# Kernel tuning notes

Hardware: AMD Instinct MI355X
Metric: run time of the kernel (lower is better)

Reference implementation:

```python
import jax, jax.numpy as jnp
import numpy as np

B, N = 64, 4096
D_IN, D_SLOT, K, N_ITER, MLP_H = 128, 128, 8, 3, 256
EPS = 1e-8
LN_EPS = 1e-5  # torch LayerNorm default


def layer_norm(x, g, b):
    m = jnp.mean(x, axis=-1, keepdims=True)
    v = jnp.mean((x - m) ** 2, axis=-1, keepdims=True)
    return (x - m) * jax.lax.rsqrt(v + LN_EPS) * g + b


def setup_inputs() -> dict:
    key = jax.random.key(0)
    ks = jax.random.split(key, 12)
    s = D_SLOT ** -0.5
    return {
        "inputs": jax.random.normal(ks[0], (B, N, D_IN), jnp.float32),
        "noise": jax.random.normal(ks[1], (B, K, D_SLOT), jnp.float32),
        "ln_in_g": jnp.ones((D_IN,), jnp.float32),
        "ln_in_b": jnp.zeros((D_IN,), jnp.float32),
        "ln_sl_g": jnp.ones((D_SLOT,), jnp.float32),
        "ln_sl_b": jnp.zeros((D_SLOT,), jnp.float32),
        "ln_mlp_g": jnp.ones((D_SLOT,), jnp.float32),
        "ln_mlp_b": jnp.zeros((D_SLOT,), jnp.float32),
        "slots_mu": jax.random.normal(ks[2], (1, 1, D_SLOT), jnp.float32) * s,
        "slots_log_sigma": jnp.zeros((1, 1, D_SLOT), jnp.float32),
        "Wq": jax.random.normal(ks[3], (D_SLOT, D_SLOT), jnp.float32) * s,
        "Wk": jax.random.normal(ks[4], (D_SLOT, D_IN), jnp.float32) * s,
        "Wv": jax.random.normal(ks[5], (D_SLOT, D_IN), jnp.float32) * s,
        "gru_Wih": jax.random.normal(ks[6], (3 * D_SLOT, D_SLOT), jnp.float32) * s,
        "gru_Whh": jax.random.normal(ks[7], (3 * D_SLOT, D_SLOT), jnp.float32) * s,
        "gru_bih": jnp.zeros((3 * D_SLOT,), jnp.float32),
        "gru_bhh": jnp.zeros((3 * D_SLOT,), jnp.float32),
        "mlp_W1": jax.random.normal(ks[8], (MLP_H, D_SLOT), jnp.float32) * s,
        "mlp_b1": jnp.zeros((MLP_H,), jnp.float32),
        "mlp_W2": jax.random.normal(ks[9], (D_SLOT, MLP_H), jnp.float32) * (MLP_H ** -0.5),
        "mlp_b2": jnp.zeros((D_SLOT,), jnp.float32),
    }


def gru_cell(x, h, Wih, Whh, bih, bhh):
    # torch GRUCell: gate order r, z, n
    gx = x @ Wih.T + bih
    gh = h @ Whh.T + bhh
    xr, xz, xn = jnp.split(gx, 3, axis=-1)
    hr, hz, hn = jnp.split(gh, 3, axis=-1)
    r = jax.nn.sigmoid(xr + hr)
    z = jax.nn.sigmoid(xz + hz)
    n = jnp.tanh(xn + r * hn)
    return (1.0 - z) * n + z * h


def reference(inputs, noise, ln_in_g, ln_in_b, ln_sl_g, ln_sl_b, ln_mlp_g, ln_mlp_b,
              slots_mu, slots_log_sigma, Wq, Wk, Wv,
              gru_Wih, gru_Whh, gru_bih, gru_bhh,
              mlp_W1, mlp_b1, mlp_W2, mlp_b2):
    # init slots: mu + sigma * eps
    slots = slots_mu + jnp.exp(slots_log_sigma) * noise  # (B, K, d)
    x = layer_norm(inputs, ln_in_g, ln_in_b)
    k = jnp.einsum('bnd,ed->bne', x, Wk)  # (B, N, d_slot)
    v = jnp.einsum('bnd,ed->bne', x, Wv)
    scale = D_SLOT ** -0.5
    attn = None
    for _ in range(N_ITER):
        slots_prev = slots
        s_n = layer_norm(slots, ln_sl_g, ln_sl_b)
        q = jnp.einsum('bkd,ed->bke', s_n, Wq)
        dots = jnp.einsum('bkd,bnd->bkn', q, k) * scale
        attn = jax.nn.softmax(dots, axis=1)  # competitive: softmax over slots
        attn_normed = attn / (jnp.sum(attn, axis=-1, keepdims=True) + EPS)
        updates = jnp.einsum('bkn,bnd->bkd', attn_normed, v)
        slots = gru_cell(updates.reshape(-1, D_SLOT), slots_prev.reshape(-1, D_SLOT),
                         gru_Wih, gru_Whh, gru_bih, gru_bhh).reshape(B, K, D_SLOT)
        h = layer_norm(slots, ln_mlp_g, ln_mlp_b)
        h = jax.nn.gelu(h @ mlp_W1.T + mlp_b1, approximate=False)
        slots = slots + h @ mlp_W2.T + mlp_b2
    return slots, attn
```

## Files before the change

kernel.cpp:

```cpp
#include <hip/hip_runtime.h>
#include <hip/hip_bf16.h>
#include <math.h>

typedef unsigned int u32;
typedef unsigned long long u64;
typedef unsigned short u16;
typedef __bf16 bf16x8 __attribute__((ext_vector_type(8)));
typedef float f32x4 __attribute__((ext_vector_type(4)));

#define DEV __device__ __forceinline__

DEV u32 bfr(float f){ u32 u = __float_as_uint(f); return (u + 0x7fffu + ((u>>16)&1u)) >> 16; }
DEV u16 b1v(float a){ return __builtin_bit_cast(u16, (__bf16)a); }
DEV u32 pk2(float a, float b){
  return (u32)__builtin_bit_cast(u16, (__bf16)a) | ((u32)__builtin_bit_cast(u16, (__bf16)b) << 16);
}
DEV float red32(float v){
  v += __shfl_xor(v,1); v += __shfl_xor(v,2); v += __shfl_xor(v,4);
  v += __shfl_xor(v,8); v += __shfl_xor(v,16); return v;
}

__global__ void kInitSlots(const float* __restrict__ noise, const float* __restrict__ mu,
                           const float* __restrict__ ls, float* __restrict__ slots){
  int i4 = blockIdx.x*256 + threadIdx.x;
  int d4 = i4 & 31;
  float4 nv = ((const float4*)noise)[i4];
  float4 mv = ((const float4*)mu)[d4];
  float4 lv = ((const float4*)ls)[d4];
  float4 r;
  r.x = mv.x + expf(lv.x)*nv.x;
  r.y = mv.y + expf(lv.y)*nv.y;
  r.z = mv.z + expf(lv.z)*nv.z;
  r.w = mv.w + expf(lv.w)*nv.w;
  ((float4*)slots)[i4] = r;
}

__global__ void kInitW(const float* __restrict__ Wk, const float* __restrict__ Wv,
                       const float* __restrict__ g, const float* __restrict__ bb,
                       u16* __restrict__ wg, float* __restrict__ c1, float* __restrict__ c2){
  int e = threadIdx.x;
  const float4* src = (const float4*)((e < 128) ? (Wk + e*128) : (Wv + (e-128)*128));
  float a1 = 0.f, a2 = 0.f;
  #pragma unroll
  for (int d4 = 0; d4 < 32; ++d4){
    float4 wv = src[d4];
    float4 gv = ((const float4*)g)[d4];
    float4 bv = ((const float4*)bb)[d4];
    a1 += wv.x*gv.x + wv.y*gv.y + wv.z*gv.z + wv.w*gv.w;
    a2 += wv.x*bv.x + wv.y*bv.y + wv.z*bv.z + wv.w*bv.w;
    u32 w0 = bfr(wv.x*gv.x) | (bfr(wv.y*gv.y) << 16);
    u32 w1 = bfr(wv.z*gv.z) | (bfr(wv.w*gv.w) << 16);
    *(uint2*)&wg[e*128 + d4*4] = make_uint2(w0, w1);
  }
  c1[e] = a1; c2[e] = a2;
}

__global__ void kInitT(const float* __restrict__ Wih, const float* __restrict__ Whh,
                       const float* __restrict__ W1, const float* __restrict__ W2,
                       float2* __restrict__ gruT, float* __restrict__ w1T, float* __restrict__ w2T){
  int i = blockIdx.x*256 + threadIdx.x;
  if (i < 49152){
    int d = i / 384, g = i - d*384;
    gruT[i] = make_float2(Wih[g*128 + d], Whh[g*128 + d]);
  } else if (i < 81920){
    int j = i - 49152;
    int d = j >> 8, h = j & 255;
    w1T[j] = W1[h*128 + d];
  } else if (i < 114688){
    int q = i - 81920;
    int j = q >> 7, d = q & 127;
    w2T[q] = W2[d*256 + j];
  }
}

__global__ __launch_bounds__(512, 2) void kA(const float* __restrict__ x,
    const u16* __restrict__ wg, const float* __restrict__ c1g, const float* __restrict__ c2g,
    u16* __restrict__ kbuf, u16* __restrict__ vbuf)
{
  __shared__ __align__(16) u16 sWg[128*128];
  __shared__ __align__(16) u16 sE[8*16*128];
  __shared__ float sC1[128], sC2[128];
  const int t = threadIdx.x, l = t & 63, w = t >> 6;
  const int bid = blockIdx.x;
  const int half = (bid >> 3) & 1;
  const int rowgroup = (bid & 7)*32 + (bid >> 4);
  const int rowbase = rowgroup * 1024;

  const uint4* wg4 = (const uint4*)wg;
  #pragma unroll
  for (int p = 0; p < 4; ++p){
    int G = t + p*512;
    int row = G >> 4, g = G & 15;
    uint4 v = wg4[(half*128 + row)*16 + g];
    *(uint4*)&sWg[row*128 + ((g ^ (row & 7)) << 3)] = v;
  }
  if (t < 128){ sC1[t] = c1g[half*128 + t]; sC2[t] = c2g[half*128 + t]; }
  __syncthreads();

  u16* dstbuf = half ? vbuf : kbuf;
  const float4* x4 = (const float4*)x;

  #pragma unroll 1
  for (int s = 0; s < 8; ++s){
    const int r0 = rowbase + s*128 + w*16;
    const int myrow = r0 + (l & 15);
    float s1 = 0.f, s2 = 0.f;
    uint4 af[4];
    #pragma unroll
    for (int kt = 0; kt < 4; ++kt){
      int g = kt*4 + (l >> 4);
      float4 A = x4[(size_t)myrow*32 + g*2];
      float4 B = x4[(size_t)myrow*32 + g*2 + 1];
      s1 += A.x + A.y + A.z + A.w + B.x + B.y + B.z + B.w;
      s2 += A.x*A.x + A.y*A.y + A.z*A.z + A.w*A.w
          + B.x*B.x + B.y*B.y + B.z*B.z + B.w*B.w;
      af[kt].x = pk2(A.x, A.y);
      af[kt].y = pk2(A.z, A.w);
      af[kt].z = pk2(B.x, B.y);
      af[kt].w = pk2(B.z, B.w);
    }
    s1 += __shfl_xor(s1, 16); s2 += __shfl_xor(s2, 16);
    s1 += __shfl_xor(s1, 32); s2 += __shfl_xor(s2, 32);
    float m = s1 * 0.0078125f;
    float rstd = rsqrtf(s2 * 0.0078125f - m*m + 1e-5f);
    f32x4 acc[8];
    #pragma unroll
    for (int c_ = 0; c_ < 8; ++c_) acc[c_] = (f32x4){0.f,0.f,0.f,0.f};
    #pragma unroll
    for (int ct = 0; ct < 8; ++ct){
      uint4 bf[4];
      #pragma unroll
      for (int kt = 0; kt < 4; ++kt){
        int wr = ct*16 + (l & 15);
        int g = kt*4 + (l >> 4);
        bf[kt] = *(const uint4*)&sWg[wr*128 + ((g ^ (wr & 7)) << 3)];
      }
      #pragma unroll
      for (int kt = 0; kt < 4; ++kt)
        acc[ct] = __builtin_amdgcn_mfma_f32_16x16x32_bf16(
            __builtin_bit_cast(bf16x8, af[kt]),
            __builtin_bit_cast(bf16x8, bf[kt]),
            acc[ct], 0, 0, 0);
    }
    float mvp[4], rvp[4];
    #pragma unroll
    for (int r = 0; r < 4; ++r){
      int rl = (l >> 4)*4 + r;
      mvp[r] = __shfl(m, rl);
      rvp[r] = __shfl(rstd, rl);
    }
    #pragma unroll
    for (int ct = 0; ct < 8; ++ct){
      int col = ct*16 + (l & 15);
      float c1v = sC1[col], c2v = sC2[col];
      #pragma unroll
      for (int r = 0; r < 4; ++r){
        int rl = (l >> 4)*4 + r;
        float valf = rvp[r]*(acc[ct][r] - mvp[r]*c1v) + c2v;
        int gran = (col >> 3) ^ (rl & 7);
        sE[w*2048 + rl*128 + (gran << 3) + (col & 7)] = b1v(valf);
      }
    }
    uint4* dst4 = (uint4*)dstbuf;
    #pragma unroll
    for (int p = 0; p < 4; ++p){
      int fl = l + p*64;
      int nl = fl >> 4, gb = fl & 15;
      uint4 v = *(const uint4*)&sE[w*2048 + nl*128 + ((gb ^ (nl & 7)) << 3)];
      dst4[(size_t)(r0 + nl)*16 + gb] = v;
    }
  }
}

__global__ __launch_bounds__(256) void kQ(const float* __restrict__ slots,
    const float* __restrict__ Wq, const float* __restrict__ lng, const float* __restrict__ lnb,
    uint4* __restrict__ qg)
{
  const int b = blockIdx.x, t = threadIdx.x;
  const int k8 = t >> 5, q32 = t & 31;
  __shared__ __align__(16) float sSn[1024];
  __shared__ __align__(16) float sQ[1024];
  {
    float4 sv = ((const float4*)slots)[b*256 + t];
    float s  = sv.x + sv.y + sv.z + sv.w;
    float ss = sv.x*sv.x + sv.y*sv.y + sv.z*sv.z + sv.w*sv.w;
    s = red32(s); ss = red32(ss);
    float m = s*0.0078125f, var = ss*0.0078125f - m*m;
    float rstd = rsqrtf(var + 1e-5f);
    float4 gv = ((const float4*)lng)[q32], bv = ((const float4*)lnb)[q32];
    float4 sn;
    sn.x = (sv.x - m)*rstd*gv.x + bv.x;
    sn.y = (sv.y - m)*rstd*gv.y + bv.y;
    sn.z = (sv.z - m)*rstd*gv.z + bv.z;
    sn.w = (sv.w - m)*rstd*gv.w + bv.w;
    *(float4*)&sSn[t*4] = sn;
  }
  __syncthreads();
  {
    const float4* Wq4 = (const float4*)Wq;
    #pragma unroll
    for (int i = 0; i < 4; ++i){
      int e = i*32 + q32;
      float acc = 0.f;
      #pragma unroll
      for (int d4 = 0; d4 < 32; ++d4){
        float4 qs = *(const float4*)&sSn[k8*128 + d4*4];
        float4 wv = Wq4[e*32 + d4];
        acc = fmaf(qs.x,wv.x,acc); acc = fmaf(qs.y,wv.y,acc);
        acc = fmaf(qs.z,wv.z,acc); acc = fmaf(qs.w,wv.w,acc);
      }
      sQ[k8*128 + e] = acc * 0.08838834764831845f;
    }
  }
  __syncthreads();
  if (t < 128){
    int slot = t >> 4, g = t & 15;
    const float* src = &sQ[slot*128 + g*8];
    uint4 o;
    o.x = pk2(src[0], src[1]); o.y = pk2(src[2], src[3]);
    o.z = pk2(src[4], src[5]); o.w = pk2(src[6], src[7]);
    qg[(b*8 + slot)*16 + g] = o;
  }
}

__global__ __launch_bounds__(256) void kB(const u16* __restrict__ kbuf,
   const u16* __restrict__ vbuf, const uint4* __restrict__ qg,
   float* __restrict__ part, float* __restrict__ attn_out, int write_attn,
   int cshift, int ntiles)
{
  const int t = threadIdx.x;
  const int b = blockIdx.x >> cshift, chunk = blockIdx.x & ((1 << cshift) - 1);
  const int w = t >> 6, l = t & 63;
  __shared__ __align__(16) u16 sVT[128*64];
  __shared__ __align__(16) u16 sAttnB[16*64];
  __shared__ float sRsP[32];

  uint4 qf[4];
  {
    int slot = l & 15;
    uint4 z = make_uint4(0,0,0,0);
    qf[0] = z; qf[1] = z; qf[2] = z; qf[3] = z;
    if (slot < 8){
      const uint4* qb = qg + ((size_t)b*8 + slot)*16 + (l >> 4);
      #pragma unroll
      for (int kt = 0; kt < 4; ++kt) qf[kt] = qb[kt*4];
    }
  }

  f32x4 accPV0 = (f32x4){0.f,0.f,0.f,0.f};
  f32x4 accPV1 = (f32x4){0.f,0.f,0.f,0.f};
  float rs = 0.f;
  const int myrow = w*16 + (l & 15);
  const size_t base = (size_t)b*4096 + (size_t)chunk*(ntiles*64);

  uint4 kf[4];
  {
    const u16* kr = kbuf + (base + myrow)*128;
    #pragma unroll
    for (int kt = 0; kt < 4; ++kt) kf[kt] = *(const uint4*)(kr + (kt*4 + (l >> 4))*8);
  }

  #pragma unroll 1
  for (int tile = 0; tile < ntiles; ++tile){
    const int n0 = tile*64;
    uint4 vld[4];
    {
      const uint4* vg = (const uint4*)(vbuf + (base + n0)*128);
      #pragma unroll
      for (int p = 0; p < 4; ++p) vld[p] = vg[t + p*256];
    }
    f32x4 dacc = (f32x4){0.f,0.f,0.f,0.f};
    #pragma unroll
    for (int kt = 0; kt < 4; ++kt)
      dacc = __builtin_amdgcn_mfma_f32_16x16x32_bf16(
          __builtin_bit_cast(bf16x8, kf[kt]),
          __builtin_bit_cast(bf16x8, qf[kt]), dacc, 0, 0, 0);
    if (tile < ntiles - 1){
      const u16* kr = kbuf + (base + n0 + 64 + myrow)*128;
      #pragma unroll
      for (int kt = 0; kt < 4; ++kt) kf[kt] = *(const uint4*)(kr + (kt*4 + (l >> 4))*8);
    }
    float at[4];
    #pragma unroll
    for (int r = 0; r < 4; ++r){
      float d = dacc[r];
      float mx = fmaxf(d, __shfl_xor(d, 1));
      mx = fmaxf(mx, __shfl_xor(mx, 2));
      mx = fmaxf(mx, __shfl_xor(mx, 4));
      float e = expf(d - mx);
      float ssum = e + __shfl_xor(e, 1);
      ssum += __shfl_xor(ssum, 2);
      ssum += __shfl_xor(ssum, 4);
      at[r] = e / ssum;
      rs += at[r];
    }
    {
      int slot = l & 15;
      int nb = w*16 + (l >> 4)*4;
      int g = (nb >> 3) ^ (slot & 7);
      *(u64*)((char*)sAttnB + slot*128 + (g << 4) + ((nb & 7) << 1)) =
          ((u64)pk2(at[2], at[3]) << 32) | (u64)pk2(at[0], at[1]);
    }
    #pragma unroll
    for (int p = 0; p < 4; ++p){
      int fl = t + p*256;
      int nl = fl >> 4, gb = fl & 15;
      u32 arr[4] = {vld[p].x, vld[p].y, vld[p].z, vld[p].w};
      #pragma unroll
      for (int h = 0; h < 4; ++h){
        #pragma unroll
        for (int e2 = 0; e2 < 2; ++e2){
          int e = h*2 + e2;
          int d = gb*8 + e;
          int g = (nl >> 3) ^ (d & 7) ^ (gb & 7);
          *(u16*)((char*)sVT + d*128 + (g << 4) + ((nl & 7) << 1)) =
              (u16)(e2 ? (arr[h] >> 16) : (arr[h] & 0xffffu));
        }
      }
    }
    __syncthreads();
    #pragma unroll
    for (int step = 0; step < 2; ++step){
      uint4 paf;
      {
        int slot = l & 15;
        int g = (step*4 + (l >> 4)) ^ (slot & 7);
        paf = *(const uint4*)((const char*)sAttnB + slot*128 + (g << 4));
      }
      #pragma unroll
      for (int ct = 0; ct < 2; ++ct){
        int d = w*32 + ct*16 + (l & 15);
        int g = (step*4 + (l >> 4)) ^ (d & 7) ^ ((d >> 3) & 7);
        uint4 pbf = *(const uint4*)((const char*)sVT + d*128 + (g << 4));
        if (ct == 0)
          accPV0 = __builtin_amdgcn_mfma_f32_16x16x32_bf16(
              __builtin_bit_cast(bf16x8, paf), __builtin_bit_cast(bf16x8, pbf), accPV0, 0,0,0);
        else
          accPV1 = __builtin_amdgcn_mfma_f32_16x16x32_bf16(
              __builtin_bit_cast(bf16x8, paf), __builtin_bit_cast(bf16x8, pbf), accPV1, 0,0,0);
      }
    }
    if (write_attn && (l & 15) < 8){
      #pragma unroll
      for (int r = 0; r < 4; ++r)
        attn_out[(size_t)(b*8 + (l & 15))*4096 + chunk*(ntiles*64) + n0 + w*16 + (l >> 4)*4 + r] = at[r];
    }
    __syncthreads();
  }

  float* pb = part + (size_t)blockIdx.x*1040;
  if ((l >> 4) < 2){
    #pragma unroll
    for (int r = 0; r < 4; ++r){
      int slot = (l >> 4)*4 + r;
      pb[slot*128 + w*32 + (l & 15)] = accPV0[r];
      pb[slot*128 + w*32 + 16 + (l & 15)] = accPV1[r];
    }
  }
  rs += __shfl_xor(rs, 16);
  rs += __shfl_xor(rs, 32);
  if (l < 8) sRsP[w*8 + l] = rs;
  __syncthreads();
  if (t < 8) pb[1024 + t] = sRsP[t] + sRsP[8 + t] + sRsP[16 + t] + sRsP[24 + t];
}

__global__ __launch_bounds__(384) void kC(const float* __restrict__ part,
  float* __restrict__ slots, const float2* __restrict__ gruT,
  const float* __restrict__ bih, const float* __restrict__ bhh,
  const float* __restrict__ lng, const float* __restrict__ lnb,
  const float* __restrict__ w1T, const float* __restrict__ b1,
  const float* __restrict__ w2T, const float* __restrict__ b2,
  float* __restrict__ out_slots, int last, int nchunk)
{
  const int t = threadIdx.x;
  const int r = blockIdx.x, b = r >> 3, k = r & 7;
  __shared__ float sU[128], sS[128], sG1[384], sG2[384];
  __shared__ float sNew[128], sH[128], sH1[256];
  __shared__ float sP[4];

  if (t < 128){
    float rs = 1e-8f;
    for (int c = 0; c < nchunk; ++c) rs += part[(size_t)(b*nchunk + c)*1040 + 1024 + k];
    float u = 0.f;
    for (int c = 0; c < nchunk; ++c) u += part[(size_t)(b*nchunk + c)*1040 + k*128 + t];
    sU[t] = u / rs;
    sS[t] = slots[r*128 + t];
  }
  __syncthreads();

  {
    float acc1 = bih[t], acc2 = bhh[t];
    #pragma unroll 8
    for (int d = 0; d < 128; ++d){
      float2 w = gruT[d*384 + t];
      float ud = sU[d], sd = sS[d];
      acc1 = fmaf(ud, w.x, acc1);
      acc2 = fmaf(sd, w.y, acc2);
    }
    sG1[t] = acc1; sG2[t] = acc2;
  }
  __syncthreads();

  if (t < 128){
    float rr = 1.f/(1.f + expf(-(sG1[t] + sG2[t])));
    float zz = 1.f/(1.f + expf(-(sG1[128 + t] + sG2[128 + t])));
    float nn = tanhf(sG1[256 + t] + rr*sG2[256 + t]);
    sNew[t] = (1.f - zz)*nn + zz*sS[t];
  }
  __syncthreads();
  if (t < 128){
    float v = sNew[t];
    float s = v, ss = v*v;
    s  += __shfl_xor(s,1);  ss += __shfl_xor(ss,1);
    s  += __shfl_xor(s,2);  ss += __shfl_xor(ss,2);
    s  += __shfl_xor(s,4);  ss += __shfl_xor(ss,4);
    s  += __shfl_xor(s,8);  ss += __shfl_xor(ss,8);
    s  += __shfl_xor(s,16); ss += __shfl_xor(ss,16);
    s  += __shfl_xor(s,32); ss += __shfl_xor(ss,32);
    if ((t & 63) == 0){ sP[(t >> 6)*2] = s; sP[(t >> 6)*2 + 1] = ss; }
  }
  __syncthreads();
  if (t < 128){
    float s = sP[0] + sP[2], ss = sP[1] + sP[3];
    float m = s*0.0078125f, var = ss*0.0078125f - m*m;
    float rstd = rsqrtf(var + 1e-5f);
    sH[t] = (sNew[t] - m)*rstd*lng[t] + lnb[t];
  }
  __syncthreads();

  if (t < 256){
    float acc = b1[t];
    #pragma unroll 8
    for (int d = 0; d < 128; ++d)
      acc = fmaf(sH[d], w1T[d*256 + t], acc);
    sH1[t] = 0.5f*acc*(1.f + erff(acc*0.70710678118654752f));
  }
  __syncthreads();

  if (t < 128){
    float acc = b2[t];
    #pragma unroll 8
    for (int j = 0; j < 256; ++j)
      acc = fmaf(sH1[j], w2T[j*128 + t], acc);
    float res = sNew[t] + acc;
    slots[r*128 + t] = res;
    if (last) out_slots[r*128 + t] = res;
  }
}

extern "C" void kernel_launch(void* const* d_in, const int* in_sizes, int n_in,
                              void* d_out, int out_size, void* d_ws, size_t ws_size,
                              hipStream_t stream)
{
  const float* inputs   = (const float*)d_in[0];
  const float* noise    = (const float*)d_in[1];
  const float* ln_in_g  = (const float*)d_in[2];
  const float* ln_in_b  = (const float*)d_in[3];
  const float* ln_sl_g  = (const float*)d_in[4];
  const float* ln_sl_b  = (const float*)d_in[5];
  const float* ln_mlp_g = (const float*)d_in[6];
  const float* ln_mlp_b = (const float*)d_in[7];
  const float* slots_mu = (const float*)d_in[8];
  const float* slots_ls = (const float*)d_in[9];
  const float* Wq  = (const float*)d_in[10];
  const float* Wk  = (const float*)d_in[11];
  const float* Wv  = (const float*)d_in[12];
  const float* Wih = (const float*)d_in[13];
  const float* Whh = (const float*)d_in[14];
  const float* bih = (const float*)d_in[15];
  const float* bhh = (const float*)d_in[16];
  const float* W1  = (const float*)d_in[17];
  const float* b1  = (const float*)d_in[18];
  const float* W2  = (const float*)d_in[19];
  const float* b2  = (const float*)d_in[20];
  float* out = (float*)d_out;

  char* ws = (char*)d_ws;
  u16*   kbuf  = (u16*)ws;
  u16*   vbuf  = (u16*)(ws + 67108864);
  float* slots = (float*)(ws + 134217728);
  u16*   wg    = (u16*)(ws + 134479872);
  float* c1    = (float*)(ws + 134545408);
  float* c2    = (float*)(ws + 134546432);
  float* part  = (float*)(ws + 134547456);

  int cshift, nchunk;
  {
    size_t need16 = 134547456ull + 16ull*64*1040*4 + 393216 + 131072 + 131072 + 131072;
    if (ws_size >= need16){ cshift = 4; nchunk = 16; }
    else                  { cshift = 3; nchunk = 8;  }
  }
  size_t partB = (size_t)nchunk*64*1040*4;
  float2* gruT = (float2*)(ws + 134547456 + partB);
  float*  w1T  = (float*)(ws + 134547456 + partB + 393216);
  float*  w2T  = (float*)(ws + 134547456 + partB + 393216 + 131072);
  uint4*  qg   = (uint4*)(ws + 134547456 + partB + 393216 + 262144);
  int ntiles = 64 / nchunk;

  kInitSlots<<<64, 256, 0, stream>>>(noise, slots_mu, slots_ls, slots);
  kInitW<<<1, 256, 0, stream>>>(Wk, Wv, ln_in_g, ln_in_b, wg, c1, c2);
  kInitT<<<448, 256, 0, stream>>>(Wih, Whh, W1, W2, gruT, w1T, w2T);
  kA<<<512, 512, 0, stream>>>(inputs, wg, c1, c2, kbuf, vbuf);
  for (int it = 0; it < 3; ++it){
    kQ<<<64, 256, 0, stream>>>(slots, Wq, ln_sl_g, ln_sl_b, qg);
    kB<<<64*nchunk, 256, 0, stream>>>(kbuf, vbuf, qg, part, out + 65536,
                                      it == 2, cshift, ntiles);
    kC<<<512, 384, 0, stream>>>(part, slots, gruT, bih, bhh,
                                ln_mlp_g, ln_mlp_b, w1T, b1, w2T, b2, out, it == 2, nchunk);
  }
}
```

Measured before the change: 342.1 us.

## Fuse next-iteration query projection into kC, prefetch V tiles, split kA blocks

kA now runs twice as many blocks, each handling half of a rowgroup's sub-tiles, to raise parallelism. kB prefetches the next V tile into registers alongside the next K tile and moves the attention writes before the barrier. kC now also computes the LayerNorm and Wq projection for the next iteration's queries, removing two of the three kQ launches. The costs are more register pressure in kB, a per-row Wq read in each kC block, and kA reloading its weight tile twice as often.

```diff
diff --git a/kernel.cpp b/kernel.cpp
--- a/kernel.cpp
+++ b/kernel.cpp
@@ -83,7 +83,8 @@
   const int t = threadIdx.x, l = t & 63, w = t >> 6;
   const int bid = blockIdx.x;
   const int half = (bid >> 3) & 1;
-  const int rowgroup = (bid & 7)*32 + (bid >> 4);
+  const int sub  = (bid >> 4) & 1;
+  const int rowgroup = (bid & 7)*32 + (bid >> 5);
   const int rowbase = rowgroup * 1024;
 
   const uint4* wg4 = (const uint4*)wg;
@@ -101,7 +102,7 @@
   const float4* x4 = (const float4*)x;
 
   #pragma unroll 1
-  for (int s = 0; s < 8; ++s){
+  for (int s = sub*4; s < sub*4 + 4; ++s){
     const int r0 = rowbase + s*128 + w*16;
     const int myrow = r0 + (l & 15);
     float s1 = 0.f, s2 = 0.f;
@@ -253,32 +254,33 @@
   const int myrow = w*16 + (l & 15);
   const size_t base = (size_t)b*4096 + (size_t)chunk*(ntiles*64);
 
-  uint4 kf[4];
+  uint4 kf[4], vld[4];
   {
     const u16* kr = kbuf + (base + myrow)*128;
     #pragma unroll
     for (int kt = 0; kt < 4; ++kt) kf[kt] = *(const uint4*)(kr + (kt*4 + (l >> 4))*8);
+    const uint4* vg = (const uint4*)(vbuf + base*128);
+    #pragma unroll
+    for (int p = 0; p < 4; ++p) vld[p] = vg[t + p*256];
   }
 
   #pragma unroll 1
   for (int tile = 0; tile < ntiles; ++tile){
     const int n0 = tile*64;
-    uint4 vld[4];
-    {
-      const uint4* vg = (const uint4*)(vbuf + (base + n0)*128);
-      #pragma unroll
-      for (int p = 0; p < 4; ++p) vld[p] = vg[t + p*256];
-    }
     f32x4 dacc = (f32x4){0.f,0.f,0.f,0.f};
     #pragma unroll
     for (int kt = 0; kt < 4; ++kt)
       dacc = __builtin_amdgcn_mfma_f32_16x16x32_bf16(
           __builtin_bit_cast(bf16x8, kf[kt]),
           __builtin_bit_cast(bf16x8, qf[kt]), dacc, 0, 0, 0);
+    uint4 vldN[4];
     if (tile < ntiles - 1){
       const u16* kr = kbuf + (base + n0 + 64 + myrow)*128;
       #pragma unroll
       for (int kt = 0; kt < 4; ++kt) kf[kt] = *(const uint4*)(kr + (kt*4 + (l >> 4))*8);
+      const uint4* vg = (const uint4*)(vbuf + (base + n0 + 64)*128);
+      #pragma unroll
+      for (int p = 0; p < 4; ++p) vldN[p] = vg[t + p*256];
     }
     float at[4];
     #pragma unroll
@@ -318,6 +320,11 @@
         }
       }
     }
+    if (write_attn && (l & 15) < 8){
+      #pragma unroll
+      for (int r = 0; r < 4; ++r)
+        attn_out[(size_t)(b*8 + (l & 15))*4096 + chunk*(ntiles*64) + n0 + w*16 + (l >> 4)*4 + r] = at[r];
+    }
     __syncthreads();
     #pragma unroll
     for (int step = 0; step < 2; ++step){
@@ -340,12 +347,11 @@
               __builtin_bit_cast(bf16x8, paf), __builtin_bit_cast(bf16x8, pbf), accPV1, 0,0,0);
       }
     }
-    if (write_attn && (l & 15) < 8){
-      #pragma unroll
-      for (int r = 0; r < 4; ++r)
-        attn_out[(size_t)(b*8 + (l & 15))*4096 + chunk*(ntiles*64) + n0 + w*16 + (l >> 4)*4 + r] = at[r];
-    }
     __syncthreads();
+    if (tile < ntiles - 1){
+      #pragma unroll
+      for (int p = 0; p < 4; ++p) vld[p] = vldN[p];
+    }
   }
 
   float* pb = part + (size_t)blockIdx.x*1040;
@@ -370,6 +376,8 @@
   const float* __restrict__ lng, const float* __restrict__ lnb,
   const float* __restrict__ w1T, const float* __restrict__ b1,
   const float* __restrict__ w2T, const float* __restrict__ b2,
+  const float* __restrict__ lnslg, const float* __restrict__ lnslb,
+  const float* __restrict__ Wq, uint4* __restrict__ qg,
   float* __restrict__ out_slots, int last, int nchunk)
 {
   const int t = threadIdx.x;
@@ -437,14 +445,59 @@
   }
   __syncthreads();
 
+  float res = 0.f;
   if (t < 128){
     float acc = b2[t];
     #pragma unroll 8
     for (int j = 0; j < 256; ++j)
       acc = fmaf(sH1[j], w2T[j*128 + t], acc);
-    float res = sNew[t] + acc;
+    res = sNew[t] + acc;
     slots[r*128 + t] = res;
     if (last) out_slots[r*128 + t] = res;
+  }
+  if (last) return;
+
+  __syncthreads();
+  if (t < 128) sH[t] = res;
+  __syncthreads();
+  if (t < 128){
+    float v = sH[t];
+    float s = v, ss = v*v;
+    s  += __shfl_xor(s,1);  ss += __shfl_xor(ss,1);
+    s  += __shfl_xor(s,2);  ss += __shfl_xor(ss,2);
+    s  += __shfl_xor(s,4);  ss += __shfl_xor(ss,4);
+    s  += __shfl_xor(s,8);  ss += __shfl_xor(ss,8);
+    s  += __shfl_xor(s,16); ss += __shfl_xor(ss,16);
+    s  += __shfl_xor(s,32); ss += __shfl_xor(ss,32);
+    if ((t & 63) == 0){ sP[(t >> 6)*2] = s; sP[(t >> 6)*2 + 1] = ss; }
+  }
+  __syncthreads();
+  if (t < 128){
+    float s = sP[0] + sP[2], ss = sP[1] + sP[3];
+    float m = s*0.0078125f, var = ss*0.0078125f - m*m;
+    float rstd = rsqrtf(var + 1e-5f);
+    sU[t] = (sH[t] - m)*rstd*lnslg[t] + lnslb[t];
+  }
+  __syncthreads();
+  if (t < 128){
+    const float4* Wq4 = (const float4*)Wq;
+    float acc = 0.f;
+    #pragma unroll 8
+    for (int d4 = 0; d4 < 32; ++d4){
+      float4 wv = Wq4[t*32 + d4];
+      float4 hv = *(const float4*)&sU[d4*4];
+      acc = fmaf(wv.x,hv.x,acc); acc = fmaf(wv.y,hv.y,acc);
+      acc = fmaf(wv.z,hv.z,acc); acc = fmaf(wv.w,hv.w,acc);
+    }
+    sG1[t] = acc * 0.08838834764831845f;
+  }
+  __syncthreads();
+  if (t < 16){
+    const float* src = &sG1[t*8];
+    uint4 o;
+    o.x = pk2(src[0], src[1]); o.y = pk2(src[2], src[3]);
+    o.z = pk2(src[4], src[5]); o.w = pk2(src[6], src[7]);
+    qg[(size_t)r*16 + t] = o;
   }
 }
 
@@ -500,12 +553,13 @@
   kInitSlots<<<64, 256, 0, stream>>>(noise, slots_mu, slots_ls, slots);
   kInitW<<<1, 256, 0, stream>>>(Wk, Wv, ln_in_g, ln_in_b, wg, c1, c2);
   kInitT<<<448, 256, 0, stream>>>(Wih, Whh, W1, W2, gruT, w1T, w2T);
-  kA<<<512, 512, 0, stream>>>(inputs, wg, c1, c2, kbuf, vbuf);
+  kA<<<1024, 512, 0, stream>>>(inputs, wg, c1, c2, kbuf, vbuf);
+  kQ<<<64, 256, 0, stream>>>(slots, Wq, ln_sl_g, ln_sl_b, qg);
   for (int it = 0; it < 3; ++it){
-    kQ<<<64, 256, 0, stream>>>(slots, Wq, ln_sl_g, ln_sl_b, qg);
     kB<<<64*nchunk, 256, 0, stream>>>(kbuf, vbuf, qg, part, out + 65536,
                                       it == 2, cshift, ntiles);
     kC<<<512, 384, 0, stream>>>(part, slots, gruT, bih, bhh,
-                                ln_mlp_g, ln_mlp_b, w1T, b1, w2T, b2, out, it == 2, nchunk);
-  }
-}
+                                ln_mlp_g, ln_mlp_b, w1T, b1, w2T, b2,
+                                ln_sl_g, ln_sl_b, Wq, qg, out, it == 2, nchunk);
+  }
+}
```

Result: faster. 317.8 us (-7.1%).
